# Kernel tuning notes

Measured on AMD Instinct MI355X. Metric: run time of the kernel, lower is better.

## Reference

```python
import jax, jax.numpy as jnp
import numpy as np

NEG_SLOPE = 0.2  # LeakyReLU slope from the torch module


def setup_inputs() -> dict:
    key = jax.random.key(0)
    k1, k2, k3 = jax.random.split(key, 3)
    B, N, IN = 32, 512, 256
    H, D = 8, 32  # out_dim=256, concat=True -> head_dim = 256 // 8
    x = jax.random.normal(k1, (B, N, IN), dtype=jnp.float32)
    # nn.Linear(in_dim, H*D, bias=False).weight has shape (H*D, in_dim)
    W = jax.random.normal(k2, (H * D, IN), dtype=jnp.float32) * (1.0 / np.sqrt(IN))
    # xavier_uniform on (1, H, 2D)
    limit = float(np.sqrt(6.0 / (H + 2 * D)))
    attn = jax.random.uniform(k3, (1, H, 2 * D), dtype=jnp.float32, minval=-limit, maxval=limit)
    return {"x": x, "W": W, "attn": attn}


def reference(x, W, attn):
    # x: (B, N, IN); W: (H*D, IN); attn: (1, H, 2D)
    B, N, _ = x.shape
    H = attn.shape[1]
    D = attn.shape[2] // 2
    Wx = (x @ W.T).reshape(B, N, H, D)  # (B, N, H, D)
    # Additive attention decomposes: e[b,i,j,h] = leaky(s_src[b,i,h] + s_tgt[b,j,h]).
    # (src = Wx broadcast over j, tgt = Wx broadcast over i; cat*attn sums split in two.)
    a_src = attn[0, :, :D]  # (H, D)
    a_tgt = attn[0, :, D:]  # (H, D)
    s_src = jnp.einsum('bnhd,hd->bnh', Wx, a_src)
    s_tgt = jnp.einsum('bnhd,hd->bnh', Wx, a_tgt)
    e = jax.nn.leaky_relu(s_src[:, :, None, :] + s_tgt[:, None, :, :], NEG_SLOPE)  # (B,N,N,H)
    a = jax.nn.softmax(e, axis=2)  # softmax over source nodes j
    # dropout p=0 (eval mode) -> identity
    out = jnp.einsum('bijh,bjhd->bihd', a, Wx)  # (B, N, H, D)
    out = out.reshape(B, N, H * D)  # concat=True
    return jax.nn.elu(out)
```

## Files before the change

kernel.cpp:

```cpp
#include <hip/hip_runtime.h>
#include <math.h>

#define NEG_SLOPE 0.2f
#define LOG2E 1.44269504088896f

typedef _Float16 f16x8 __attribute__((ext_vector_type(8)));
typedef float f32x4 __attribute__((ext_vector_type(4)));

union PK8 { uint4 u4; _Float16 h[8]; };
union PK4 { uint2 u2; _Float16 h[4]; };
union PK1 { unsigned short u; _Float16 h; };

__global__ __launch_bounds__(512) void gat_fused(const float* __restrict__ x,
                                                 const float* __restrict__ W,
                                                 const float* __restrict__ attn,
                                                 float* __restrict__ out) {
    __shared__ __align__(16) unsigned short Ws[32 * 256];
    __shared__ __align__(16) unsigned short Xs[512 * 64];
    __shared__ __align__(16) unsigned short wxt[32 * 512];
    __shared__ float stf[512];
    __shared__ float ssrc[512];
    __shared__ float red_s[8];

    const int bid = blockIdx.x;
    const int b = bid & 31, h = bid >> 5;
    const int tid = threadIdx.x;
    const int w = tid >> 6, l = tid & 63;
    const int q = l >> 4, ln = l & 15;

    float av_s[2][4], av_t[2][4];
    #pragma unroll
    for (int dt = 0; dt < 2; ++dt)
        #pragma unroll
        for (int r = 0; r < 4; ++r) {
            int d = dt * 16 + q * 4 + r;
            av_s[dt][r] = attn[h * 64 + d];
            av_t[dt][r] = attn[h * 64 + 32 + d];
        }

    #pragma unroll
    for (int p = 0; p < 4; ++p) {
        int idx = p * 512 + tid;
        int d = idx >> 6, kq = idx & 63;
        float4 v = *(const float4*)(W + (size_t)(h * 32 + d) * 256 + kq * 4);
        PK4 pk;
        pk.h[0] = (_Float16)v.x; pk.h[1] = (_Float16)v.y;
        pk.h[2] = (_Float16)v.z; pk.h[3] = (_Float16)v.w;
        *(uint2*)((char*)Ws + ((d * 512 + kq * 8) ^ ((d & 7) << 4))) = pk.u2;
    }

    f32x4 gacc[2][4];
    #pragma unroll
    for (int dt = 0; dt < 2; ++dt)
        #pragma unroll
        for (int jt = 0; jt < 4; ++jt) gacc[dt][jt] = (f32x4){0.f, 0.f, 0.f, 0.f};

    const float* xb = x + (size_t)b * 512 * 256;
    for (int c4 = 0; c4 < 4; ++c4) {
        __syncthreads();
        #pragma unroll
        for (int pp = 0; pp < 4; ++pp) {
            int j = pp * 128 + (tid >> 2);
            int kseg = (tid & 3) * 16;
            const float* src = xb + (size_t)j * 256 + c4 * 64 + kseg;
            float4 v0 = *(const float4*)(src + 0);
            float4 v1 = *(const float4*)(src + 4);
            float4 v2 = *(const float4*)(src + 8);
            float4 v3 = *(const float4*)(src + 12);
            PK8 p0, p1;
            p0.h[0] = (_Float16)v0.x; p0.h[1] = (_Float16)v0.y;
            p0.h[2] = (_Float16)v0.z; p0.h[3] = (_Float16)v0.w;
            p0.h[4] = (_Float16)v1.x; p0.h[5] = (_Float16)v1.y;
            p0.h[6] = (_Float16)v1.z; p0.h[7] = (_Float16)v1.w;
            p1.h[0] = (_Float16)v2.x; p1.h[1] = (_Float16)v2.y;
            p1.h[2] = (_Float16)v2.z; p1.h[3] = (_Float16)v2.w;
            p1.h[4] = (_Float16)v3.x; p1.h[5] = (_Float16)v3.y;
            p1.h[6] = (_Float16)v3.z; p1.h[7] = (_Float16)v3.w;
            int base = j * 128 + kseg * 2;
            *(uint4*)((char*)Xs + ((base) ^ ((j & 7) << 4))) = p0.u4;
            *(uint4*)((char*)Xs + ((base + 16) ^ ((j & 7) << 4))) = p1.u4;
        }
        __syncthreads();
        #pragma unroll
        for (int ks = 0; ks < 2; ++ks) {
            f16x8 af[2];
            #pragma unroll
            for (int dt = 0; dt < 2; ++dt) {
                int d = dt * 16 + ln;
                int bb = d * 512 + c4 * 128 + ks * 64 + q * 16;
                uint4 raw = *(const uint4*)((const char*)Ws + (bb ^ ((d & 7) << 4)));
                PK8 pk; pk.u4 = raw;
                af[dt] = *(f16x8*)&pk;
            }
            #pragma unroll
            for (int jt = 0; jt < 4; ++jt) {
                int j = w * 64 + jt * 16 + ln;
                int bb = j * 128 + ks * 64 + q * 16;
                uint4 raw = *(const uint4*)((const char*)Xs + (bb ^ ((j & 7) << 4)));
                PK8 pk; pk.u4 = raw;
                f16x8 bf = *(f16x8*)&pk;
                gacc[0][jt] = __builtin_amdgcn_mfma_f32_16x16x32_f16(af[0], bf, gacc[0][jt], 0, 0, 0);
                gacc[1][jt] = __builtin_amdgcn_mfma_f32_16x16x32_f16(af[1], bf, gacc[1][jt], 0, 0, 0);
            }
        }
    }

    #pragma unroll
    for (int jt = 0; jt < 4; ++jt) {
        float ps = 0.f, pt = 0.f;
        #pragma unroll
        for (int dt = 0; dt < 2; ++dt)
            #pragma unroll
            for (int r = 0; r < 4; ++r) {
                float v = gacc[dt][jt][r];
                ps += v * av_s[dt][r];
                pt += v * av_t[dt][r];
            }
        ps += __shfl_xor(ps, 16); ps += __shfl_xor(ps, 32);
        pt += __shfl_xor(pt, 16); pt += __shfl_xor(pt, 32);
        int j = w * 64 + jt * 16 + ln;
        if (q == 0) { ssrc[j] = ps * LOG2E; stf[j] = pt * LOG2E; }
        #pragma unroll
        for (int dt = 0; dt < 2; ++dt)
            #pragma unroll
            for (int r = 0; r < 4; ++r) {
                int d = dt * 16 + q * 4 + r;
                PK1 hv; hv.h = (_Float16)gacc[dt][jt][r];
                *(unsigned short*)((char*)wxt + (((d << 10) + j * 2) ^ ((d & 7) << 4))) = hv.u;
            }
    }
    __syncthreads();

    {
        float m = stf[tid];
        #pragma unroll
        for (int off = 32; off > 0; off >>= 1)
            m = fmaxf(m, __shfl_xor(m, off));
        if (l == 0) red_s[w] = m;
    }
    __syncthreads();
    float maxtK = red_s[0];
    #pragma unroll
    for (int ww = 1; ww < 8; ++ww) maxtK = fmaxf(maxtK, red_s[ww]);

    float ciK[4], miK[4];
    #pragma unroll
    for (int g = 0; g < 4; ++g) {
        int i = w * 64 + g * 16 + ln;
        float cc = ssrc[i];
        float c = cc + maxtK;
        miK[g] = fmaxf(c, NEG_SLOPE * c);
        ciK[g] = cc;
    }

    f32x4 acc[4][2];
    #pragma unroll
    for (int g = 0; g < 4; ++g) {
        acc[g][0] = (f32x4){0.f, 0.f, 0.f, 0.f};
        acc[g][1] = (f32x4){0.f, 0.f, 0.f, 0.f};
    }
    float pd[4] = {0.f, 0.f, 0.f, 0.f};

    for (int kk = 0; kk < 16; ++kk) {
        const int j0 = kk * 32 + q * 8;
        float4 s0 = *(const float4*)(stf + j0);
        float4 s1 = *(const float4*)(stf + j0 + 4);
        float st[8] = {s0.x, s0.y, s0.z, s0.w, s1.x, s1.y, s1.z, s1.w};

        f16x8 bf[2];
        #pragma unroll
        for (int dt = 0; dt < 2; ++dt) {
            int d = dt * 16 + ln;
            int bb = d * 1024 + kk * 64 + q * 16;
            uint4 raw = *(const uint4*)((const char*)wxt + (bb ^ ((d & 7) << 4)));
            PK8 pk; pk.u4 = raw;
            bf[dt] = *(f16x8*)&pk;
        }

        #pragma unroll
        for (int g = 0; g < 4; ++g) {
            f16x8 pa;
            float s = 0.f;
            #pragma unroll
            for (int e = 0; e < 8; ++e) {
                float eK = ciK[g] + st[e];
                float lr = fmaxf(eK, NEG_SLOPE * eK);
                float p = exp2f(lr - miK[g]);
                s += p;
                pa[e] = (_Float16)p;
            }
            pd[g] += s;
            acc[g][0] = __builtin_amdgcn_mfma_f32_16x16x32_f16(pa, bf[0], acc[g][0], 0, 0, 0);
            acc[g][1] = __builtin_amdgcn_mfma_f32_16x16x32_f16(pa, bf[1], acc[g][1], 0, 0, 0);
        }
    }

    float inv[4];
    #pragma unroll
    for (int g = 0; g < 4; ++g) {
        float s = pd[g];
        s += __shfl_xor(s, 16);
        s += __shfl_xor(s, 32);
        inv[g] = 1.f / s;
    }
    #pragma unroll
    for (int g = 0; g < 4; ++g)
        #pragma unroll
        for (int dt = 0; dt < 2; ++dt)
            #pragma unroll
            for (int r = 0; r < 4; ++r) {
                int row = q * 4 + r;
                float dn = __shfl(inv[g], row);
                float o = acc[g][dt][r] * dn;
                o = o > 0.f ? o : (__expf(o) - 1.f);
                size_t i = (size_t)(b * 512 + w * 64 + g * 16 + row);
                out[i * 256 + h * 32 + dt * 16 + ln] = o;
            }
}

extern "C" void kernel_launch(void* const* d_in, const int* in_sizes, int n_in,
                              void* d_out, int out_size, void* d_ws, size_t ws_size,
                              hipStream_t stream) {
    const float* x    = (const float*)d_in[0];
    const float* W    = (const float*)d_in[1];
    const float* attn = (const float*)d_in[2];
    float* out = (float*)d_out;

    gat_fused<<<256, 512, 0, stream>>>(x, W, attn, out);
}
```

Baseline: 42.87 us.

## Split query rows across two blocks and alias shared buffers to cut LDS

The grid doubles to 512 blocks so each (batch, head) pair gets two blocks, each handling half of the query rows in the attention phase. Both blocks still recompute the full Wx projection for all 512 nodes. Shared memory shrinks because Xs, now staged 32 columns at a time over 8 chunks, shares storage with wxt, and stf/ssrc sit in the same pool, which should allow more blocks per CU. The cost is a duplicated projection GEMM and duplicated x reads per pair, plus twice as many chunk barriers and an extra sync before the aliased buffer is overwritten.

```diff
diff --git a/kernel.cpp b/kernel.cpp
--- a/kernel.cpp
+++ b/kernel.cpp
@@ -16,14 +16,16 @@
                                                  const float* __restrict__ attn,
                                                  float* __restrict__ out) {
     __shared__ __align__(16) unsigned short Ws[32 * 256];
-    __shared__ __align__(16) unsigned short Xs[512 * 64];
-    __shared__ __align__(16) unsigned short wxt[32 * 512];
-    __shared__ float stf[512];
-    __shared__ float ssrc[512];
+    __shared__ __align__(16) unsigned char pool[36 * 1024];
     __shared__ float red_s[8];
 
+    unsigned short* Xs  = (unsigned short*)pool;
+    unsigned short* wxt = (unsigned short*)pool;
+    float* stf  = (float*)(pool + 32 * 1024);
+    float* ssrc = (float*)(pool + 34 * 1024);
+
     const int bid = blockIdx.x;
-    const int b = bid & 31, h = bid >> 5;
+    const int b = bid & 31, h = (bid >> 5) & 7, half = bid >> 8;
     const int tid = threadIdx.x;
     const int w = tid >> 6, l = tid & 63;
     const int q = l >> 4, ln = l & 15;
@@ -56,13 +58,13 @@
         for (int jt = 0; jt < 4; ++jt) gacc[dt][jt] = (f32x4){0.f, 0.f, 0.f, 0.f};
 
     const float* xb = x + (size_t)b * 512 * 256;
-    for (int c4 = 0; c4 < 4; ++c4) {
+    for (int c = 0; c < 8; ++c) {
         __syncthreads();
         #pragma unroll
-        for (int pp = 0; pp < 4; ++pp) {
-            int j = pp * 128 + (tid >> 2);
-            int kseg = (tid & 3) * 16;
-            const float* src = xb + (size_t)j * 256 + c4 * 64 + kseg;
+        for (int pass = 0; pass < 2; ++pass) {
+            int j = pass * 256 + (tid >> 1);
+            int kh = (tid & 1) * 16;
+            const float* src = xb + (size_t)j * 256 + c * 32 + kh;
             float4 v0 = *(const float4*)(src + 0);
             float4 v1 = *(const float4*)(src + 4);
             float4 v2 = *(const float4*)(src + 8);
@@ -76,34 +78,33 @@
             p1.h[2] = (_Float16)v2.z; p1.h[3] = (_Float16)v2.w;
             p1.h[4] = (_Float16)v3.x; p1.h[5] = (_Float16)v3.y;
             p1.h[6] = (_Float16)v3.z; p1.h[7] = (_Float16)v3.w;
-            int base = j * 128 + kseg * 2;
+            int base = j * 64 + kh * 2;
             *(uint4*)((char*)Xs + ((base) ^ ((j & 7) << 4))) = p0.u4;
             *(uint4*)((char*)Xs + ((base + 16) ^ ((j & 7) << 4))) = p1.u4;
         }
         __syncthreads();
-        #pragma unroll
-        for (int ks = 0; ks < 2; ++ks) {
-            f16x8 af[2];
-            #pragma unroll
-            for (int dt = 0; dt < 2; ++dt) {
-                int d = dt * 16 + ln;
-                int bb = d * 512 + c4 * 128 + ks * 64 + q * 16;
-                uint4 raw = *(const uint4*)((const char*)Ws + (bb ^ ((d & 7) << 4)));
-                PK8 pk; pk.u4 = raw;
-                af[dt] = *(f16x8*)&pk;
-            }
-            #pragma unroll
-            for (int jt = 0; jt < 4; ++jt) {
-                int j = w * 64 + jt * 16 + ln;
-                int bb = j * 128 + ks * 64 + q * 16;
-                uint4 raw = *(const uint4*)((const char*)Xs + (bb ^ ((j & 7) << 4)));
-                PK8 pk; pk.u4 = raw;
-                f16x8 bf = *(f16x8*)&pk;
-                gacc[0][jt] = __builtin_amdgcn_mfma_f32_16x16x32_f16(af[0], bf, gacc[0][jt], 0, 0, 0);
-                gacc[1][jt] = __builtin_amdgcn_mfma_f32_16x16x32_f16(af[1], bf, gacc[1][jt], 0, 0, 0);
-            }
-        }
-    }
+        f16x8 af[2];
+        #pragma unroll
+        for (int dt = 0; dt < 2; ++dt) {
+            int d = dt * 16 + ln;
+            int bb = d * 512 + c * 64 + q * 16;
+            uint4 raw = *(const uint4*)((const char*)Ws + (bb ^ ((d & 7) << 4)));
+            PK8 pk; pk.u4 = raw;
+            af[dt] = *(f16x8*)&pk;
+        }
+        #pragma unroll
+        for (int jt = 0; jt < 4; ++jt) {
+            int j = w * 64 + jt * 16 + ln;
+            int bb = j * 64 + q * 16;
+            uint4 raw = *(const uint4*)((const char*)Xs + (bb ^ ((j & 7) << 4)));
+            PK8 pk; pk.u4 = raw;
+            f16x8 bf = *(f16x8*)&pk;
+            gacc[0][jt] = __builtin_amdgcn_mfma_f32_16x16x32_f16(af[0], bf, gacc[0][jt], 0, 0, 0);
+            gacc[1][jt] = __builtin_amdgcn_mfma_f32_16x16x32_f16(af[1], bf, gacc[1][jt], 0, 0, 0);
+        }
+    }
+
+    __syncthreads();
 
     #pragma unroll
     for (int jt = 0; jt < 4; ++jt) {
@@ -143,23 +144,23 @@
     #pragma unroll
     for (int ww = 1; ww < 8; ++ww) maxtK = fmaxf(maxtK, red_s[ww]);
 
-    float ciK[4], miK[4];
-    #pragma unroll
-    for (int g = 0; g < 4; ++g) {
-        int i = w * 64 + g * 16 + ln;
+    float ciK[2], miK[2];
+    #pragma unroll
+    for (int g = 0; g < 2; ++g) {
+        int i = half * 256 + w * 32 + g * 16 + ln;
         float cc = ssrc[i];
-        float c = cc + maxtK;
-        miK[g] = fmaxf(c, NEG_SLOPE * c);
+        float cm = cc + maxtK;
+        miK[g] = fmaxf(cm, NEG_SLOPE * cm);
         ciK[g] = cc;
     }
 
-    f32x4 acc[4][2];
-    #pragma unroll
-    for (int g = 0; g < 4; ++g) {
+    f32x4 acc[2][2];
+    #pragma unroll
+    for (int g = 0; g < 2; ++g) {
         acc[g][0] = (f32x4){0.f, 0.f, 0.f, 0.f};
         acc[g][1] = (f32x4){0.f, 0.f, 0.f, 0.f};
     }
-    float pd[4] = {0.f, 0.f, 0.f, 0.f};
+    float pd[2] = {0.f, 0.f};
 
     for (int kk = 0; kk < 16; ++kk) {
         const int j0 = kk * 32 + q * 8;
@@ -178,7 +179,7 @@
         }
 
         #pragma unroll
-        for (int g = 0; g < 4; ++g) {
+        for (int g = 0; g < 2; ++g) {
             f16x8 pa;
             float s = 0.f;
             #pragma unroll
@@ -195,16 +196,16 @@
         }
     }
 
-    float inv[4];
-    #pragma unroll
-    for (int g = 0; g < 4; ++g) {
+    float inv[2];
+    #pragma unroll
+    for (int g = 0; g < 2; ++g) {
         float s = pd[g];
         s += __shfl_xor(s, 16);
         s += __shfl_xor(s, 32);
         inv[g] = 1.f / s;
     }
     #pragma unroll
-    for (int g = 0; g < 4; ++g)
+    for (int g = 0; g < 2; ++g)
         #pragma unroll
         for (int dt = 0; dt < 2; ++dt)
             #pragma unroll
@@ -213,7 +214,7 @@
                 float dn = __shfl(inv[g], row);
                 float o = acc[g][dt][r] * dn;
                 o = o > 0.f ? o : (__expf(o) - 1.f);
-                size_t i = (size_t)(b * 512 + w * 64 + g * 16 + row);
+                size_t i = (size_t)(b * 512 + half * 256 + w * 32 + g * 16 + row);
                 out[i * 256 + h * 32 + dt * 16 + ln] = o;
             }
 }
@@ -226,5 +227,5 @@
     const float* attn = (const float*)d_in[2];
     float* out = (float*)d_out;
 
-    gat_fused<<<256, 512, 0, stream>>>(x, W, attn, out);
+    gat_fused<<<512, 512, 0, stream>>>(x, W, attn, out);
 }
```

Result: slower. 51.44 us (+20.0%).
